# Kernel optimization log

Measured on AMD Instinct MI355X. Metric: run time of the kernel, lower is better.

## Reference

```python
import jax, jax.numpy as jnp
import numpy as np

NUM_EDGES = 1_600_000
HIDDEN = 128
NUM_SEGMENTS = 256


def setup_inputs() -> dict:
    key = jax.random.key(0)
    k1, k2, k3, k4, k5 = jax.random.split(key, 5)
    x = jax.random.normal(k1, (NUM_EDGES, HIDDEN), dtype=jnp.float32)
    batch_indices = jnp.sort(
        jax.random.randint(k2, (NUM_EDGES,), 0, NUM_SEGMENTS, dtype=jnp.int32)
    )
    # Linear layer params (PyTorch-style fan-in init scale).
    s = 1.0 / np.sqrt(HIDDEN)
    W1 = jax.random.uniform(k3, (HIDDEN, HIDDEN), jnp.float32, -s, s)
    b1 = jax.random.uniform(k4, (HIDDEN,), jnp.float32, -s, s)
    w2 = jax.random.uniform(k5, (HIDDEN,), jnp.float32, -s, s)
    b2 = jnp.zeros((), jnp.float32)
    return {"x": x, "batch_indices": batch_indices, "W1": W1, "b1": b1, "w2": w2, "b2": b2}


def reference(x, batch_indices, W1, b1, w2, b2):
    # attention_linear + relu (dropout is identity in eval mode)
    feats = jax.nn.relu(x @ W1.T + b1)          # [E, H]
    scores = feats @ w2 + b2                    # [E]  (score_linear squeezed)
    # per-segment numerically-stable softmax over ragged segments
    seg_max = jax.ops.segment_max(scores, batch_indices, num_segments=NUM_SEGMENTS)
    e = jnp.exp(scores - seg_max[batch_indices])             # [E]
    denom = jax.ops.segment_sum(e, batch_indices, num_segments=NUM_SEGMENTS)  # [B]
    weights = e / denom[batch_indices]                       # [E]
    # weighted segment sum; empty segments naturally yield zeros
    pooled = jax.ops.segment_sum(x * weights[:, None], batch_indices,
                                 num_segments=NUM_SEGMENTS)  # [B, H]
    return pooled
```

## Files before the change

### kernel.cpp

```cpp
#include <hip/hip_runtime.h>
#include <hip/hip_bf16.h>


#define H 128
#define NBLK 1024
#define WPB 4
#define NW (NBLK * WPB)

typedef __attribute__((ext_vector_type(8))) __bf16 bf16x8;
typedef __attribute__((ext_vector_type(4))) float f32x4;

__global__ void gat_init(const float* __restrict__ W1, float* __restrict__ num,
                         float* __restrict__ denom, unsigned short* __restrict__ w1bf,
                         int nseg) {
    int i = blockIdx.x * 256 + threadIdx.x;
    if (i < nseg * H) num[i] = 0.0f;
    if (i < nseg) denom[i] = 0.0f;
    if (i < H * H) {
        int j = i >> 7;
        float f = W1[i];
        unsigned int u = __float_as_uint(f);
        unsigned short b = (unsigned short)((u + 0x7fffu + ((u >> 16) & 1u)) >> 16);
        int dst = i ^ ((j & 7) << 3);
        w1bf[dst] = b;
    }
}

__global__ __launch_bounds__(256, 2) void gat_main(
    const float* __restrict__ x, const int* __restrict__ bi,
    const unsigned short* __restrict__ w1bf, const float* __restrict__ b1,
    const float* __restrict__ w2, const float* __restrict__ b2p,
    float* __restrict__ num, float* __restrict__ denom, int E) {

    __shared__ uint4 ldsW[2048];

    const int t = threadIdx.x;
    const int lane = t & 63;
    const int lr = lane & 15;
    const int lg = lane >> 4;

    const uint4* w1v = (const uint4*)w1bf;
#pragma unroll
    for (int k = 0; k < 8; ++k) ldsW[k * 256 + t] = w1v[k * 256 + t];

    float b1v[8], w2v[8];
#pragma unroll
    for (int nf = 0; nf < 8; ++nf) { b1v[nf] = b1[nf * 16 + lr]; w2v[nf] = w2[nf * 16 + lr]; }
    const float b2v = b2p[0];

    __syncthreads();

    const int gw = blockIdx.x * WPB + (t >> 6);
    const long rbeg = ((long)gw * E) / NW;
    const long rend = ((long)(gw + 1) * E) / NW;
    if (rbeg >= rend) return;
    const int nch = (int)((rend - rbeg + 15) >> 4);

    const float4* x4 = (const float4*)x;

    float v[32];
#pragma unroll
    for (int i = 0; i < 32; ++i) v[i] = 0.0f;
    float dsum = 0.0f;

    auto flush = [&](int seg) {
        {
            const bool h0 = lr & 1;
#pragma unroll
            for (int j = 0; j < 16; ++j) {
                float send = h0 ? v[j] : v[j + 16];
                float recv = __shfl_xor(send, 1, 64);
                v[j] = (h0 ? v[j + 16] : v[j]) + recv;
            }
            const bool h1 = lr & 2;
#pragma unroll
            for (int j = 0; j < 8; ++j) {
                float send = h1 ? v[j] : v[j + 8];
                float recv = __shfl_xor(send, 2, 64);
                v[j] = (h1 ? v[j + 8] : v[j]) + recv;
            }
            const bool h2 = lr & 4;
#pragma unroll
            for (int j = 0; j < 4; ++j) {
                float send = h2 ? v[j] : v[j + 4];
                float recv = __shfl_xor(send, 4, 64);
                v[j] = (h2 ? v[j + 4] : v[j]) + recv;
            }
            const bool h3 = lr & 8;
#pragma unroll
            for (int j = 0; j < 2; ++j) {
                float send = h3 ? v[j] : v[j + 2];
                float recv = __shfl_xor(send, 8, 64);
                v[j] = (h3 ? v[j + 2] : v[j]) + recv;
            }
        }
        int i0 = ((lr & 1) << 4) | ((lr & 2) << 2) | (lr & 4) | ((lr & 8) >> 2);
        int col0 = (i0 >> 3) * 32 + lg * 8 + (i0 & 7);
        atomicAdd(&num[seg * H + col0], v[0]);
        atomicAdd(&num[seg * H + col0 + 1], v[1]);
        float d = dsum;
#pragma unroll
        for (int m = 1; m <= 32; m <<= 1) d += __shfl_xor(d, m, 64);
        if (lane == 0) atomicAdd(&denom[seg], d * 0.25f);
#pragma unroll
        for (int i = 0; i < 32; ++i) v[i] = 0.0f;
        dsum = 0.0f;
    };

    int cur = bi[rbeg];

    for (int c = 0; c < nch; c += 2) {
        const long rA = rbeg + (long)c * 16 + lr;
        const long rB = rA + 16;
        const long rcA = rA < rend ? rA : rend - 1;
        const long rcB = rB < rend ? rB : rend - 1;
        const bool validA = rA < rend;
        const bool validB = rB < rend;

        const float4* pA = x4 + rcA * 32 + lg * 2;
        const float4* pB = x4 + rcB * 32 + lg * 2;
        bf16x8 afA[4], afB[4];
#pragma unroll
        for (int ks = 0; ks < 4; ++ks) {
            const float4 u0 = pA[ks * 8], u1 = pA[ks * 8 + 1];
            bf16x8 a;
            a[0] = (__bf16)u0.x; a[1] = (__bf16)u0.y; a[2] = (__bf16)u0.z; a[3] = (__bf16)u0.w;
            a[4] = (__bf16)u1.x; a[5] = (__bf16)u1.y; a[6] = (__bf16)u1.z; a[7] = (__bf16)u1.w;
            afA[ks] = a;
        }
#pragma unroll
        for (int ks = 0; ks < 4; ++ks) {
            const float4 u0 = pB[ks * 8], u1 = pB[ks * 8 + 1];
            bf16x8 a;
            a[0] = (__bf16)u0.x; a[1] = (__bf16)u0.y; a[2] = (__bf16)u0.z; a[3] = (__bf16)u0.w;
            a[4] = (__bf16)u1.x; a[5] = (__bf16)u1.y; a[6] = (__bf16)u1.z; a[7] = (__bf16)u1.w;
            afB[ks] = a;
        }
        const int msA = bi[rcA];
        const int msB = bi[rcB];

        float scA[4] = {0.f, 0.f, 0.f, 0.f};
        float scB[4] = {0.f, 0.f, 0.f, 0.f};
#pragma unroll
        for (int nf = 0; nf < 8; ++nf) {
            f32x4 accA = (f32x4)0.0f, accB = (f32x4)0.0f;
#pragma unroll
            for (int ks = 0; ks < 4; ++ks) {
                int j = nf * 16 + lr;
                int chunk = (j * 16 + ks * 4 + lg) ^ (j & 7);
                bf16x8 bb = __builtin_bit_cast(bf16x8, ldsW[chunk]);
                accA = __builtin_amdgcn_mfma_f32_16x16x32_bf16(afA[ks], bb, accA, 0, 0, 0);
                accB = __builtin_amdgcn_mfma_f32_16x16x32_bf16(afB[ks], bb, accB, 0, 0, 0);
            }
            const float bv = b1v[nf], wv = w2v[nf];
#pragma unroll
            for (int r4 = 0; r4 < 4; ++r4) {
                scA[r4] = fmaf(fmaxf(accA[r4] + bv, 0.0f), wv, scA[r4]);
                scB[r4] = fmaf(fmaxf(accB[r4] + bv, 0.0f), wv, scB[r4]);
            }
        }
#pragma unroll
        for (int m = 1; m <= 8; m <<= 1)
#pragma unroll
            for (int r4 = 0; r4 < 4; ++r4) {
                scA[r4] += __shfl_xor(scA[r4], m, 64);
                scB[r4] += __shfl_xor(scB[r4], m, 64);
            }

        const int src = ((lr >> 2) << 4) | lr;
        float s4A[4], s4B[4];
#pragma unroll
        for (int r4 = 0; r4 < 4; ++r4) {
            s4A[r4] = __shfl(scA[r4], src, 64);
            s4B[r4] = __shfl(scB[r4], src, 64);
        }
        const int rsel = lr & 3;
        const float sA = rsel == 0 ? s4A[0] : rsel == 1 ? s4A[1] : rsel == 2 ? s4A[2] : s4A[3];
        const float sB = rsel == 0 ? s4B[0] : rsel == 1 ? s4B[1] : rsel == 2 ? s4B[2] : s4B[3];
        const float eA = validA ? __expf(sA + b2v) : 0.0f;
        const float eB = validB ? __expf(sB + b2v) : 0.0f;

        while (true) {
            const bool mine = validA && (msA == cur);
            const float em = mine ? eA : 0.0f;
#pragma unroll
            for (int ks = 0; ks < 4; ++ks)
#pragma unroll
                for (int el = 0; el < 8; ++el)
                    v[ks * 8 + el] = fmaf(em, (float)afA[ks][el], v[ks * 8 + el]);
            dsum += em;
            unsigned long long rest = __ballot(validA && msA > cur);
            if (!rest) break;
            flush(cur);
            int idx = __ffsll(rest) - 1;
            cur = __shfl(msA, idx, 64);
        }
        while (true) {
            const bool mine = validB && (msB == cur);
            const float em = mine ? eB : 0.0f;
#pragma unroll
            for (int ks = 0; ks < 4; ++ks)
#pragma unroll
                for (int el = 0; el < 8; ++el)
                    v[ks * 8 + el] = fmaf(em, (float)afB[ks][el], v[ks * 8 + el]);
            dsum += em;
            unsigned long long rest = __ballot(validB && msB > cur);
            if (!rest) break;
            flush(cur);
            int idx = __ffsll(rest) - 1;
            cur = __shfl(msB, idx, 64);
        }
    }
    flush(cur);
}

__global__ void gat_fin(const float* __restrict__ num, const float* __restrict__ denom,
                        float* __restrict__ out, int n) {
    int i = blockIdx.x * 256 + threadIdx.x;
    if (i < n) {
        float d = denom[i >> 7];
        out[i] = (d > 0.0f) ? num[i] / d : 0.0f;
    }
}

extern "C" void kernel_launch(void* const* d_in, const int* in_sizes, int n_in,
                              void* d_out, int out_size, void* d_ws, size_t ws_size,
                              hipStream_t stream) {
    const float* x  = (const float*)d_in[0];
    const int*   bi = (const int*)d_in[1];
    const float* W1 = (const float*)d_in[2];
    const float* b1 = (const float*)d_in[3];
    const float* w2 = (const float*)d_in[4];
    const float* b2 = (const float*)d_in[5];
    const int E = in_sizes[1];
    const int nseg = out_size / H;

    float* num = (float*)d_ws;
    float* denom = num + (size_t)nseg * H;
    unsigned short* w1bf = (unsigned short*)(denom + nseg);

    int initN = nseg * H > H * H ? nseg * H : H * H;
    gat_init<<<(initN + 255) / 256, 256, 0, stream>>>(W1, num, denom, w1bf, nseg);
    gat_main<<<NBLK, 256, 0, stream>>>(x, bi, w1bf, b1, w2, b2, num, denom, E);
    gat_fin<<<(out_size + 255) / 256, 256, 0, stream>>>(num, denom, (float*)d_out, out_size);
}
```

Measured before the change: 189.3 us.

## Software-prefetch next row pair into registers and halve block count

Loads for the next two 16-row chunks of x and their segment indices are now issued into a 16-entry float4 register buffer before the current chunk's MFMA work, so global-memory latency overlaps with compute. The grid is also halved to 512 blocks, giving each wave twice as many rows. The prefetch buffer adds 64 VGPRs, which can lower occupancy, and fewer blocks means fewer waves in flight to hide latency.

```diff
diff --git a/kernel.cpp b/kernel.cpp
--- a/kernel.cpp
+++ b/kernel.cpp
@@ -3,7 +3,7 @@
 
 
 #define H 128
-#define NBLK 1024
+#define NBLK 512
 #define WPB 4
 #define NW (NBLK * WPB)
 
@@ -107,37 +107,48 @@
         dsum = 0.0f;
     };
 
-    int cur = bi[rbeg];
-
-    for (int c = 0; c < nch; c += 2) {
+    float4 pf[16];
+    int msA_p, msB_p;
+    auto issue = [&](int c) {
         const long rA = rbeg + (long)c * 16 + lr;
         const long rB = rA + 16;
         const long rcA = rA < rend ? rA : rend - 1;
         const long rcB = rB < rend ? rB : rend - 1;
-        const bool validA = rA < rend;
-        const bool validB = rB < rend;
-
         const float4* pA = x4 + rcA * 32 + lg * 2;
         const float4* pB = x4 + rcB * 32 + lg * 2;
+#pragma unroll
+        for (int ks = 0; ks < 4; ++ks) {
+            pf[ks * 2]         = pA[ks * 8];
+            pf[ks * 2 + 1]     = pA[ks * 8 + 1];
+            pf[8 + ks * 2]     = pB[ks * 8];
+            pf[8 + ks * 2 + 1] = pB[ks * 8 + 1];
+        }
+        msA_p = bi[rcA];
+        msB_p = bi[rcB];
+    };
+
+    int cur = bi[rbeg];
+    issue(0);
+
+    for (int c = 0; c < nch; c += 2) {
+        const bool validA = (rbeg + (long)c * 16 + lr) < rend;
+        const bool validB = (rbeg + (long)(c + 1) * 16 + lr) < rend;
+        const int msA = msA_p, msB = msB_p;
+
         bf16x8 afA[4], afB[4];
 #pragma unroll
         for (int ks = 0; ks < 4; ++ks) {
-            const float4 u0 = pA[ks * 8], u1 = pA[ks * 8 + 1];
-            bf16x8 a;
+            const float4 u0 = pf[ks * 2], u1 = pf[ks * 2 + 1];
+            const float4 w0 = pf[8 + ks * 2], w1 = pf[8 + ks * 2 + 1];
+            bf16x8 a, b;
             a[0] = (__bf16)u0.x; a[1] = (__bf16)u0.y; a[2] = (__bf16)u0.z; a[3] = (__bf16)u0.w;
             a[4] = (__bf16)u1.x; a[5] = (__bf16)u1.y; a[6] = (__bf16)u1.z; a[7] = (__bf16)u1.w;
-            afA[ks] = a;
-        }
-#pragma unroll
-        for (int ks = 0; ks < 4; ++ks) {
-            const float4 u0 = pB[ks * 8], u1 = pB[ks * 8 + 1];
-            bf16x8 a;
-            a[0] = (__bf16)u0.x; a[1] = (__bf16)u0.y; a[2] = (__bf16)u0.z; a[3] = (__bf16)u0.w;
-            a[4] = (__bf16)u1.x; a[5] = (__bf16)u1.y; a[6] = (__bf16)u1.z; a[7] = (__bf16)u1.w;
-            afB[ks] = a;
-        }
-        const int msA = bi[rcA];
-        const int msB = bi[rcB];
+            b[0] = (__bf16)w0.x; b[1] = (__bf16)w0.y; b[2] = (__bf16)w0.z; b[3] = (__bf16)w0.w;
+            b[4] = (__bf16)w1.x; b[5] = (__bf16)w1.y; b[6] = (__bf16)w1.z; b[7] = (__bf16)w1.w;
+            afA[ks] = a; afB[ks] = b;
+        }
+
+        if (c + 2 < nch) issue(c + 2);
 
         float scA[4] = {0.f, 0.f, 0.f, 0.f};
         float scB[4] = {0.f, 0.f, 0.f, 0.f};
```

Result: slower. 326.1 us (+72.3%).

## Process four row tiles per iteration and prefetch next pair during MFMA

Applied to the files above, without the earlier changes.

The main loop now handles four 16-row tiles per iteration instead of two. Global loads for tiles C and D are issued into a register buffer before the MFMA work on tiles A and B, so the memory latency overlaps with compute. This is a software-pipelining change meant to hide HBM load latency in a bandwidth-bound kernel. It raises register pressure (extra fragments, a 16-entry float4 buffer, more score accumulators), which may reduce occupancy or cause spills.

```diff
diff --git a/kernel.cpp b/kernel.cpp
--- a/kernel.cpp
+++ b/kernel.cpp
@@ -109,35 +109,50 @@
 
     int cur = bi[rbeg];
 
-    for (int c = 0; c < nch; c += 2) {
+    for (int c = 0; c < nch; c += 4) {
         const long rA = rbeg + (long)c * 16 + lr;
-        const long rB = rA + 16;
+        const long rB = rA + 16, rC = rA + 32, rD = rA + 48;
         const long rcA = rA < rend ? rA : rend - 1;
         const long rcB = rB < rend ? rB : rend - 1;
-        const bool validA = rA < rend;
-        const bool validB = rB < rend;
+        const long rcC = rC < rend ? rC : rend - 1;
+        const long rcD = rD < rend ? rD : rend - 1;
+        const bool vA = rA < rend, vB = rB < rend, vC = rC < rend, vD = rD < rend;
 
         const float4* pA = x4 + rcA * 32 + lg * 2;
         const float4* pB = x4 + rcB * 32 + lg * 2;
+        float4 q[16];
+#pragma unroll
+        for (int ks = 0; ks < 4; ++ks) {
+            q[ks * 2]         = pA[ks * 8];
+            q[ks * 2 + 1]     = pA[ks * 8 + 1];
+            q[8 + ks * 2]     = pB[ks * 8];
+            q[8 + ks * 2 + 1] = pB[ks * 8 + 1];
+        }
+        const int msA = bi[rcA], msB = bi[rcB];
+
         bf16x8 afA[4], afB[4];
 #pragma unroll
         for (int ks = 0; ks < 4; ++ks) {
-            const float4 u0 = pA[ks * 8], u1 = pA[ks * 8 + 1];
-            bf16x8 a;
+            const float4 u0 = q[ks * 2], u1 = q[ks * 2 + 1];
+            const float4 w0 = q[8 + ks * 2], w1 = q[8 + ks * 2 + 1];
+            bf16x8 a, b;
             a[0] = (__bf16)u0.x; a[1] = (__bf16)u0.y; a[2] = (__bf16)u0.z; a[3] = (__bf16)u0.w;
             a[4] = (__bf16)u1.x; a[5] = (__bf16)u1.y; a[6] = (__bf16)u1.z; a[7] = (__bf16)u1.w;
-            afA[ks] = a;
-        }
+            b[0] = (__bf16)w0.x; b[1] = (__bf16)w0.y; b[2] = (__bf16)w0.z; b[3] = (__bf16)w0.w;
+            b[4] = (__bf16)w1.x; b[5] = (__bf16)w1.y; b[6] = (__bf16)w1.z; b[7] = (__bf16)w1.w;
+            afA[ks] = a; afB[ks] = b;
+        }
+
+        const float4* pC = x4 + rcC * 32 + lg * 2;
+        const float4* pD = x4 + rcD * 32 + lg * 2;
 #pragma unroll
         for (int ks = 0; ks < 4; ++ks) {
-            const float4 u0 = pB[ks * 8], u1 = pB[ks * 8 + 1];
-            bf16x8 a;
-            a[0] = (__bf16)u0.x; a[1] = (__bf16)u0.y; a[2] = (__bf16)u0.z; a[3] = (__bf16)u0.w;
-            a[4] = (__bf16)u1.x; a[5] = (__bf16)u1.y; a[6] = (__bf16)u1.z; a[7] = (__bf16)u1.w;
-            afB[ks] = a;
-        }
-        const int msA = bi[rcA];
-        const int msB = bi[rcB];
+            q[ks * 2]         = pC[ks * 8];
+            q[ks * 2 + 1]     = pC[ks * 8 + 1];
+            q[8 + ks * 2]     = pD[ks * 8];
+            q[8 + ks * 2 + 1] = pD[ks * 8 + 1];
+        }
+        const int msC = bi[rcC], msD = bi[rcD];
 
         float scA[4] = {0.f, 0.f, 0.f, 0.f};
         float scB[4] = {0.f, 0.f, 0.f, 0.f};
@@ -159,29 +174,74 @@
                 scB[r4] = fmaf(fmaxf(accB[r4] + bv, 0.0f), wv, scB[r4]);
             }
         }
+
+        bf16x8 afC[4], afD[4];
+#pragma unroll
+        for (int ks = 0; ks < 4; ++ks) {
+            const float4 u0 = q[ks * 2], u1 = q[ks * 2 + 1];
+            const float4 w0 = q[8 + ks * 2], w1 = q[8 + ks * 2 + 1];
+            bf16x8 a, b;
+            a[0] = (__bf16)u0.x; a[1] = (__bf16)u0.y; a[2] = (__bf16)u0.z; a[3] = (__bf16)u0.w;
+            a[4] = (__bf16)u1.x; a[5] = (__bf16)u1.y; a[6] = (__bf16)u1.z; a[7] = (__bf16)u1.w;
+            b[0] = (__bf16)w0.x; b[1] = (__bf16)w0.y; b[2] = (__bf16)w0.z; b[3] = (__bf16)w0.w;
+            b[4] = (__bf16)w1.x; b[5] = (__bf16)w1.y; b[6] = (__bf16)w1.z; b[7] = (__bf16)w1.w;
+            afC[ks] = a; afD[ks] = b;
+        }
+
+        float scC[4] = {0.f, 0.f, 0.f, 0.f};
+        float scD[4] = {0.f, 0.f, 0.f, 0.f};
+#pragma unroll
+        for (int nf = 0; nf < 8; ++nf) {
+            f32x4 accC = (f32x4)0.0f, accD = (f32x4)0.0f;
+#pragma unroll
+            for (int ks = 0; ks < 4; ++ks) {
+                int j = nf * 16 + lr;
+                int chunk = (j * 16 + ks * 4 + lg) ^ (j & 7);
+                bf16x8 bb = __builtin_bit_cast(bf16x8, ldsW[chunk]);
+                accC = __builtin_amdgcn_mfma_f32_16x16x32_bf16(afC[ks], bb, accC, 0, 0, 0);
+                accD = __builtin_amdgcn_mfma_f32_16x16x32_bf16(afD[ks], bb, accD, 0, 0, 0);
+            }
+            const float bv = b1v[nf], wv = w2v[nf];
+#pragma unroll
+            for (int r4 = 0; r4 < 4; ++r4) {
+                scC[r4] = fmaf(fmaxf(accC[r4] + bv, 0.0f), wv, scC[r4]);
+                scD[r4] = fmaf(fmaxf(accD[r4] + bv, 0.0f), wv, scD[r4]);
+            }
+        }
+
 #pragma unroll
         for (int m = 1; m <= 8; m <<= 1)
 #pragma unroll
             for (int r4 = 0; r4 < 4; ++r4) {
                 scA[r4] += __shfl_xor(scA[r4], m, 64);
                 scB[r4] += __shfl_xor(scB[r4], m, 64);
+                scC[r4] += __shfl_xor(scC[r4], m, 64);
+                scD[r4] += __shfl_xor(scD[r4], m, 64);
             }
 
         const int src = ((lr >> 2) << 4) | lr;
-        float s4A[4], s4B[4];
-#pragma unroll
-        for (int r4 = 0; r4 < 4; ++r4) {
-            s4A[r4] = __shfl(scA[r4], src, 64);
-            s4B[r4] = __shfl(scB[r4], src, 64);
-        }
         const int rsel = lr & 3;
-        const float sA = rsel == 0 ? s4A[0] : rsel == 1 ? s4A[1] : rsel == 2 ? s4A[2] : s4A[3];
-        const float sB = rsel == 0 ? s4B[0] : rsel == 1 ? s4B[1] : rsel == 2 ? s4B[2] : s4B[3];
-        const float eA = validA ? __expf(sA + b2v) : 0.0f;
-        const float eB = validB ? __expf(sB + b2v) : 0.0f;
+        float s4[4];
+#pragma unroll
+        for (int r4 = 0; r4 < 4; ++r4) s4[r4] = __shfl(scA[r4], src, 64);
+        float sA = rsel == 0 ? s4[0] : rsel == 1 ? s4[1] : rsel == 2 ? s4[2] : s4[3];
+#pragma unroll
+        for (int r4 = 0; r4 < 4; ++r4) s4[r4] = __shfl(scB[r4], src, 64);
+        float sB = rsel == 0 ? s4[0] : rsel == 1 ? s4[1] : rsel == 2 ? s4[2] : s4[3];
+#pragma unroll
+        for (int r4 = 0; r4 < 4; ++r4) s4[r4] = __shfl(scC[r4], src, 64);
+        float sC = rsel == 0 ? s4[0] : rsel == 1 ? s4[1] : rsel == 2 ? s4[2] : s4[3];
+#pragma unroll
+        for (int r4 = 0; r4 < 4; ++r4) s4[r4] = __shfl(scD[r4], src, 64);
+        float sD = rsel == 0 ? s4[0] : rsel == 1 ? s4[1] : rsel == 2 ? s4[2] : s4[3];
+
+        const float eA = vA ? __expf(sA + b2v) : 0.0f;
+        const float eB = vB ? __expf(sB + b2v) : 0.0f;
+        const float eC = vC ? __expf(sC + b2v) : 0.0f;
+        const float eD = vD ? __expf(sD + b2v) : 0.0f;
 
         while (true) {
-            const bool mine = validA && (msA == cur);
+            const bool mine = vA && (msA == cur);
             const float em = mine ? eA : 0.0f;
 #pragma unroll
             for (int ks = 0; ks < 4; ++ks)
@@ -189,14 +249,13 @@
                 for (int el = 0; el < 8; ++el)
                     v[ks * 8 + el] = fmaf(em, (float)afA[ks][el], v[ks * 8 + el]);
             dsum += em;
-            unsigned long long rest = __ballot(validA && msA > cur);
+            unsigned long long rest = __ballot(vA && msA > cur);
             if (!rest) break;
             flush(cur);
-            int idx = __ffsll(rest) - 1;
-            cur = __shfl(msA, idx, 64);
+            cur = __shfl(msA, __ffsll(rest) - 1, 64);
         }
         while (true) {
-            const bool mine = validB && (msB == cur);
+            const bool mine = vB && (msB == cur);
             const float em = mine ? eB : 0.0f;
 #pragma unroll
             for (int ks = 0; ks < 4; ++ks)
@@ -204,11 +263,38 @@
                 for (int el = 0; el < 8; ++el)
                     v[ks * 8 + el] = fmaf(em, (float)afB[ks][el], v[ks * 8 + el]);
             dsum += em;
-            unsigned long long rest = __ballot(validB && msB > cur);
+            unsigned long long rest = __ballot(vB && msB > cur);
             if (!rest) break;
             flush(cur);
-            int idx = __ffsll(rest) - 1;
-            cur = __shfl(msB, idx, 64);
+            cur = __shfl(msB, __ffsll(rest) - 1, 64);
+        }
+        while (true) {
+            const bool mine = vC && (msC == cur);
+            const float em = mine ? eC : 0.0f;
+#pragma unroll
+            for (int ks = 0; ks < 4; ++ks)
+#pragma unroll
+                for (int el = 0; el < 8; ++el)
+                    v[ks * 8 + el] = fmaf(em, (float)afC[ks][el], v[ks * 8 + el]);
+            dsum += em;
+            unsigned long long rest = __ballot(vC && msC > cur);
+            if (!rest) break;
+            flush(cur);
+            cur = __shfl(msC, __ffsll(rest) - 1, 64);
+        }
+        while (true) {
+            const bool mine = vD && (msD == cur);
+            const float em = mine ? eD : 0.0f;
+#pragma unroll
+            for (int ks = 0; ks < 4; ++ks)
+#pragma unroll
+                for (int el = 0; el < 8; ++el)
+                    v[ks * 8 + el] = fmaf(em, (float)afD[ks][el], v[ks * 8 + el]);
+            dsum += em;
+            unsigned long long rest = __ballot(vD && msD > cur);
+            if (!rest) break;
+            flush(cur);
+            cur = __shfl(msD, __ffsll(rest) - 1, 64);
         }
     }
     flush(cur);
```

Measured after the change: 497.4 us. +162.7%, slower.
